# Optimization experiments

Measured on AMD Instinct MI355X. Metric: run time of the kernel, lower is better.

The kernel has to match this reference:

```python
import jax, jax.numpy as jnp
import numpy as np

SEQ_LEN = 4096
D_MODEL = 1024
NUM_POLES = 64


def setup_inputs() -> dict:
    key = jax.random.key(0)
    k1, k2, k3 = jax.random.split(key, 3)
    z = jax.random.normal(k1, (SEQ_LEN,), dtype=jnp.float32)
    poles = jax.random.normal(k2, (D_MODEL, NUM_POLES), dtype=jnp.float32) * 0.1
    residues = jax.random.normal(k3, (D_MODEL, NUM_POLES), dtype=jnp.float32) * 0.01
    return {"z": z, "poles": poles, "residues": residues}


def reference(z, poles, residues):
    # z: (S,), poles/residues: (D, P) -> out: (S, D)
    # Cauchy sum: out[s, d] = sum_p residues[d, p] / (z[s] - poles[d, p])
    denom = z[:, None, None] - poles[None, :, :]          # (S, D, P)
    result = jnp.sum(residues[None, :, :] / denom, axis=-1)  # (S, D)
    return result
```

## Files before the change

kernel.cpp:

```cpp
#include <hip/hip_runtime.h>
#include <hip/hip_bf16.h>

#define S_TOTAL 4096
#define D_TOTAL 1024
#define NPOLES  64
#define S_PER_BLOCK 32
#define BLOCK 256

__device__ __forceinline__ float sanitize_finite(float x) {
    const float lim = 1.0e38f;
    const unsigned u = __float_as_uint(x);
    if ((u & 0x7f800000u) == 0x7f800000u)
        return (u & 0x80000000u) ? -lim : lim;
    return fminf(fmaxf(x, -lim), lim);
}

__global__ __launch_bounds__(BLOCK) void cauchy_rcp_kernel(
    const float* __restrict__ z,
    const float* __restrict__ poles,
    const float* __restrict__ residues,
    float* __restrict__ out)
{
    const int d  = blockIdx.y * BLOCK + threadIdx.x;
    const int s0 = blockIdx.x * S_PER_BLOCK;

    float pl[NPOLES], rs[NPOLES];
    const float* pp = poles    + (size_t)d * NPOLES;
    const float* rr = residues + (size_t)d * NPOLES;
#pragma unroll
    for (int p = 0; p < NPOLES; p += 4) {
        const float4 v = *reinterpret_cast<const float4*>(pp + p);
        pl[p + 0] = v.x; pl[p + 1] = v.y; pl[p + 2] = v.z; pl[p + 3] = v.w;
        const float4 w = *reinterpret_cast<const float4*>(rr + p);
        rs[p + 0] = w.x; rs[p + 1] = w.y; rs[p + 2] = w.z; rs[p + 3] = w.w;
    }

    for (int si = 0; si < S_PER_BLOCK; si += 4) {
        const float z0 = z[s0 + si + 0];
        const float z1 = z[s0 + si + 1];
        const float z2 = z[s0 + si + 2];
        const float z3 = z[s0 + si + 3];
        float a0 = 0.f, a1 = 0.f, a2 = 0.f, a3 = 0.f;
#pragma unroll
        for (int p = 0; p < NPOLES; ++p) {
            const float pol = pl[p];
            const float res = rs[p];
            a0 += res * __builtin_amdgcn_rcpf(z0 - pol);
            a1 += res * __builtin_amdgcn_rcpf(z1 - pol);
            a2 += res * __builtin_amdgcn_rcpf(z2 - pol);
            a3 += res * __builtin_amdgcn_rcpf(z3 - pol);
        }
        out[(size_t)(s0 + si + 0) * D_TOTAL + d] = sanitize_finite(a0);
        out[(size_t)(s0 + si + 1) * D_TOTAL + d] = sanitize_finite(a1);
        out[(size_t)(s0 + si + 2) * D_TOTAL + d] = sanitize_finite(a2);
        out[(size_t)(s0 + si + 3) * D_TOTAL + d] = sanitize_finite(a3);
    }
}

extern "C" void kernel_launch(void* const* d_in, const int* in_sizes, int n_in,
                              void* d_out, int out_size, void* d_ws, size_t ws_size,
                              hipStream_t stream) {
    const float* z        = (const float*)d_in[0];
    const float* poles    = (const float*)d_in[1];
    const float* residues = (const float*)d_in[2];
    float* out            = (float*)d_out;

    dim3 grid(S_TOTAL / S_PER_BLOCK, D_TOTAL / BLOCK);
    dim3 block(BLOCK);
    cauchy_rcp_kernel<<<grid, block, 0, stream>>>(z, poles, residues, out);
}
```

Measured before the change: 96.18 us.

## Combine pole pairs into rational terms to halve reciprocal count

Precomputes, per pair of poles, the sum, product and combined numerator coefficients, so each pair contributes (A z + B)/(z^2 - S z + P). The inner loop then needs one reciprocal per two poles instead of two, cutting the transcendental-rate work. It also adds a launch-bounds occupancy hint. Risk: precision loss from cancellation when paired poles are close or the quadratic denominator is small.

```diff
diff --git a/kernel.cpp b/kernel.cpp
--- a/kernel.cpp
+++ b/kernel.cpp
@@ -4,6 +4,7 @@
 #define S_TOTAL 4096
 #define D_TOTAL 1024
 #define NPOLES  64
+#define NPAIRS  32
 #define S_PER_BLOCK 32
 #define BLOCK 256
 
@@ -15,7 +16,7 @@
     return fminf(fmaxf(x, -lim), lim);
 }
 
-__global__ __launch_bounds__(BLOCK) void cauchy_rcp_kernel(
+__global__ __launch_bounds__(BLOCK, 2) void cauchy_pair_kernel(
     const float* __restrict__ z,
     const float* __restrict__ poles,
     const float* __restrict__ residues,
@@ -24,15 +25,22 @@
     const int d  = blockIdx.y * BLOCK + threadIdx.x;
     const int s0 = blockIdx.x * S_PER_BLOCK;
 
-    float pl[NPOLES], rs[NPOLES];
+    float cA[NPAIRS], cB[NPAIRS], cS[NPAIRS], cP[NPAIRS];
     const float* pp = poles    + (size_t)d * NPOLES;
     const float* rr = residues + (size_t)d * NPOLES;
 #pragma unroll
-    for (int p = 0; p < NPOLES; p += 4) {
-        const float4 v = *reinterpret_cast<const float4*>(pp + p);
-        pl[p + 0] = v.x; pl[p + 1] = v.y; pl[p + 2] = v.z; pl[p + 3] = v.w;
-        const float4 w = *reinterpret_cast<const float4*>(rr + p);
-        rs[p + 0] = w.x; rs[p + 1] = w.y; rs[p + 2] = w.z; rs[p + 3] = w.w;
+    for (int i = 0; i < NPOLES / 4; ++i) {
+        const float4 p4 = *reinterpret_cast<const float4*>(pp + 4 * i);
+        const float4 r4 = *reinterpret_cast<const float4*>(rr + 4 * i);
+        const int q = 2 * i;
+        cS[q + 0] = p4.x + p4.y;
+        cP[q + 0] = p4.x * p4.y;
+        cA[q + 0] = r4.x + r4.y;
+        cB[q + 0] = -fmaf(r4.x, p4.y, r4.y * p4.x);
+        cS[q + 1] = p4.z + p4.w;
+        cP[q + 1] = p4.z * p4.w;
+        cA[q + 1] = r4.z + r4.w;
+        cB[q + 1] = -fmaf(r4.z, p4.w, r4.w * p4.z);
     }
 
     for (int si = 0; si < S_PER_BLOCK; si += 4) {
@@ -42,13 +50,16 @@
         const float z3 = z[s0 + si + 3];
         float a0 = 0.f, a1 = 0.f, a2 = 0.f, a3 = 0.f;
 #pragma unroll
-        for (int p = 0; p < NPOLES; ++p) {
-            const float pol = pl[p];
-            const float res = rs[p];
-            a0 += res * __builtin_amdgcn_rcpf(z0 - pol);
-            a1 += res * __builtin_amdgcn_rcpf(z1 - pol);
-            a2 += res * __builtin_amdgcn_rcpf(z2 - pol);
-            a3 += res * __builtin_amdgcn_rcpf(z3 - pol);
+        for (int q = 0; q < NPAIRS; ++q) {
+            const float A = cA[q], B = cB[q], S = cS[q], P = cP[q];
+            {   const float den = fmaf(z0, z0 - S, P);
+                a0 = fmaf(fmaf(A, z0, B), __builtin_amdgcn_rcpf(den), a0); }
+            {   const float den = fmaf(z1, z1 - S, P);
+                a1 = fmaf(fmaf(A, z1, B), __builtin_amdgcn_rcpf(den), a1); }
+            {   const float den = fmaf(z2, z2 - S, P);
+                a2 = fmaf(fmaf(A, z2, B), __builtin_amdgcn_rcpf(den), a2); }
+            {   const float den = fmaf(z3, z3 - S, P);
+                a3 = fmaf(fmaf(A, z3, B), __builtin_amdgcn_rcpf(den), a3); }
         }
         out[(size_t)(s0 + si + 0) * D_TOTAL + d] = sanitize_finite(a0);
         out[(size_t)(s0 + si + 1) * D_TOTAL + d] = sanitize_finite(a1);
@@ -67,5 +78,5 @@
 
     dim3 grid(S_TOTAL / S_PER_BLOCK, D_TOTAL / BLOCK);
     dim3 block(BLOCK);
-    cauchy_rcp_kernel<<<grid, block, 0, stream>>>(z, poles, residues, out);
+    cauchy_pair_kernel<<<grid, block, 0, stream>>>(z, poles, residues, out);
 }
```

New measurement: 89.58 us. -6.9%, faster.

## Pair poles into rational terms staged in LDS, split poles across lanes

Applied to the files above, without the earlier changes.

Each pair of poles is combined into one rational term (A z + B)/(z^2 - S z + P), which halves the reciprocal count per output. The pair coefficients are precomputed once per block into shared memory. Each wavefront splits the 32 pairs across four lane groups and reduces the partial sums with cross-lane shuffles. Work per thread is reshaped to 8 z values at a time, with 64 d and 64 s per block. The risk is numerical: the combined denominator can cancel when the poles are close or z sits near a pole, which may hurt accuracy, and the shuffles and LDS reads add overhead.

```diff
diff --git a/kernel.cpp b/kernel.cpp
--- a/kernel.cpp
+++ b/kernel.cpp
@@ -4,8 +4,11 @@
 #define S_TOTAL 4096
 #define D_TOTAL 1024
 #define NPOLES  64
-#define S_PER_BLOCK 32
+#define NPAIRS  32
+#define D_PER_BLOCK 64
+#define S_PER_BLOCK 64
 #define BLOCK 256
+#define ZG 8
 
 __device__ __forceinline__ float sanitize_finite(float x) {
     const float lim = 1.0e38f;
@@ -15,45 +18,69 @@
     return fminf(fmaxf(x, -lim), lim);
 }
 
-__global__ __launch_bounds__(BLOCK) void cauchy_rcp_kernel(
+__global__ __launch_bounds__(BLOCK, 4) void cauchy_lds_kernel(
     const float* __restrict__ z,
     const float* __restrict__ poles,
     const float* __restrict__ residues,
     float* __restrict__ out)
 {
-    const int d  = blockIdx.y * BLOCK + threadIdx.x;
-    const int s0 = blockIdx.x * S_PER_BLOCK;
+    const int tid  = threadIdx.x;
+    const int lane = tid & 63;
+    const int w    = tid >> 6;
+    const int dl   = lane & 15;
+    const int q    = lane >> 4;
+    const int d0   = blockIdx.y * D_PER_BLOCK;
+    const int s0   = blockIdx.x * S_PER_BLOCK;
 
-    float pl[NPOLES], rs[NPOLES];
-    const float* pp = poles    + (size_t)d * NPOLES;
-    const float* rr = residues + (size_t)d * NPOLES;
+    __shared__ float4 cpair[NPAIRS][D_PER_BLOCK];
+
+    {
+        const int dF = tid & 63;
+        const int hq = tid >> 6;
+        const float* pp = poles    + (size_t)(d0 + dF) * NPOLES + hq * 16;
+        const float* rr = residues + (size_t)(d0 + dF) * NPOLES + hq * 16;
 #pragma unroll
-    for (int p = 0; p < NPOLES; p += 4) {
-        const float4 v = *reinterpret_cast<const float4*>(pp + p);
-        pl[p + 0] = v.x; pl[p + 1] = v.y; pl[p + 2] = v.z; pl[p + 3] = v.w;
-        const float4 w = *reinterpret_cast<const float4*>(rr + p);
-        rs[p + 0] = w.x; rs[p + 1] = w.y; rs[p + 2] = w.z; rs[p + 3] = w.w;
+        for (int k = 0; k < 4; ++k) {
+            const float4 p4 = *reinterpret_cast<const float4*>(pp + 4 * k);
+            const float4 r4 = *reinterpret_cast<const float4*>(rr + 4 * k);
+            const int pq = hq * 8 + 2 * k;
+            cpair[pq + 0][dF] = make_float4(r4.x + r4.y,
+                                            -fmaf(r4.x, p4.y, r4.y * p4.x),
+                                            p4.x + p4.y, p4.x * p4.y);
+            cpair[pq + 1][dF] = make_float4(r4.z + r4.w,
+                                            -fmaf(r4.z, p4.w, r4.w * p4.z),
+                                            p4.z + p4.w, p4.z * p4.w);
+        }
     }
+    __syncthreads();
 
-    for (int si = 0; si < S_PER_BLOCK; si += 4) {
-        const float z0 = z[s0 + si + 0];
-        const float z1 = z[s0 + si + 1];
-        const float z2 = z[s0 + si + 2];
-        const float z3 = z[s0 + si + 3];
+    const int myd  = d0 + w * 16 + dl;
+    const int widx = w * 16 + dl;
+
+    for (int g = 0; g < S_PER_BLOCK / ZG; ++g) {
+        const int sb = s0 + g * ZG;
+        const float z0 = z[sb + 0], z1 = z[sb + 1], z2 = z[sb + 2], z3 = z[sb + 3];
+        const float z4 = z[sb + 4], z5 = z[sb + 5], z6 = z[sb + 6], z7 = z[sb + 7];
         float a0 = 0.f, a1 = 0.f, a2 = 0.f, a3 = 0.f;
+        float a4 = 0.f, a5 = 0.f, a6 = 0.f, a7 = 0.f;
 #pragma unroll
-        for (int p = 0; p < NPOLES; ++p) {
-            const float pol = pl[p];
-            const float res = rs[p];
-            a0 += res * __builtin_amdgcn_rcpf(z0 - pol);
-            a1 += res * __builtin_amdgcn_rcpf(z1 - pol);
-            a2 += res * __builtin_amdgcn_rcpf(z2 - pol);
-            a3 += res * __builtin_amdgcn_rcpf(z3 - pol);
+        for (int k = 0; k < NPAIRS / 4; ++k) {
+            const float4 c = cpair[q * 8 + k][widx];
+            const float A = c.x, B = c.y, S = c.z, P = c.w;
+#define TERM(zz, aa)                                                        \
+            {   const float den = fmaf(zz, zz - S, P);                      \
+                aa = fmaf(fmaf(A, zz, B), __builtin_amdgcn_rcpf(den), aa); }
+            TERM(z0, a0) TERM(z1, a1) TERM(z2, a2) TERM(z3, a3)
+            TERM(z4, a4) TERM(z5, a5) TERM(z6, a6) TERM(z7, a7)
+#undef TERM
         }
-        out[(size_t)(s0 + si + 0) * D_TOTAL + d] = sanitize_finite(a0);
-        out[(size_t)(s0 + si + 1) * D_TOTAL + d] = sanitize_finite(a1);
-        out[(size_t)(s0 + si + 2) * D_TOTAL + d] = sanitize_finite(a2);
-        out[(size_t)(s0 + si + 3) * D_TOTAL + d] = sanitize_finite(a3);
+#define RED(aa) aa += __shfl_xor(aa, 16, 64); aa += __shfl_xor(aa, 32, 64);
+        RED(a0) RED(a1) RED(a2) RED(a3) RED(a4) RED(a5) RED(a6) RED(a7)
+#undef RED
+        const float v0 = (q == 0) ? a0 : (q == 1) ? a1 : (q == 2) ? a2 : a3;
+        const float v1 = (q == 0) ? a4 : (q == 1) ? a5 : (q == 2) ? a6 : a7;
+        out[(size_t)(sb + q) * D_TOTAL + myd]     = sanitize_finite(v0);
+        out[(size_t)(sb + 4 + q) * D_TOTAL + myd] = sanitize_finite(v1);
     }
 }
 
@@ -65,7 +92,7 @@
     const float* residues = (const float*)d_in[2];
     float* out            = (float*)d_out;
 
-    dim3 grid(S_TOTAL / S_PER_BLOCK, D_TOTAL / BLOCK);
+    dim3 grid(S_TOTAL / S_PER_BLOCK, D_TOTAL / D_PER_BLOCK);
     dim3 block(BLOCK);
-    cauchy_rcp_kernel<<<grid, block, 0, stream>>>(z, poles, residues, out);
+    cauchy_lds_kernel<<<grid, block, 0, stream>>>(z, poles, residues, out);
 }
```

New measurement: 88.29 us. 1.09x faster.
